# Performance work log

Hardware: AMD Instinct MI355X
Metric: run time of the kernel (lower is better)

The kernel has to match this reference:

```python
import jax, jax.numpy as jnp
import numpy as np

KSIZE = 7       # patch size
STRIDE_Q = 4    # stride_1: query patch stride
STRIDE_KV = 1   # stride_2: key/value patch stride
SCALE = 10.0    # softmax_scale


def unfold(x, k, stride, pad):
    """torch.nn.Unfold equivalent. x:[B,C,H,W] -> [B, C*k*k, L] (c-major, then kh, kw)."""
    x = jnp.pad(x, ((0, 0), (0, 0), (pad, pad), (pad, pad)))
    B, C, Hp, Wp = x.shape
    nh = (Hp - k) // stride + 1
    nw = (Wp - k) // stride + 1
    sl = lambda i, n: slice(i, i + (n - 1) * stride + 1, stride)
    # [B, C, k*k, nh, nw]
    pat = jnp.stack([x[:, :, sl(i, nh), sl(j, nw)] for i in range(k) for j in range(k)], axis=2)
    return pat.reshape(B, C * k * k, nh * nw)


def fold(p, k, stride, pad, H, W):
    """torch.nn.functional.fold equivalent (overlap-add). p:[B, C*k*k, L] -> [B,C,H,W]."""
    B, D, L = p.shape
    C = D // (k * k)
    nh = (H + 2 * pad - k) // stride + 1
    nw = (W + 2 * pad - k) // stride + 1
    p = p.reshape(B, C, k, k, nh, nw)
    out = jnp.zeros((B, C, H + 2 * pad, W + 2 * pad), p.dtype)
    sl = lambda i, n: slice(i, i + (n - 1) * stride + 1, stride)
    for i in range(k):
        for j in range(k):
            out = out.at[:, :, sl(i, nh), sl(j, nw)].add(p[:, :, i, j])
    return out[:, :, pad:pad + H, pad:pad + W]


def conv1x1(x, w, bias):
    # w: [out, in]
    return jnp.einsum('bihw,oi->bohw', x, w) + bias[None, :, None, None]


def setup_inputs() -> dict:
    key = jax.random.key(0)
    ks = jax.random.split(key, 9)
    B, Cin, H, W = 4, 64, 128, 128
    Cit = 16
    s_in = 1.0 / np.sqrt(Cin)
    s_it = 1.0 / np.sqrt(Cit)
    return {
        'b': jax.random.normal(ks[0], (B, Cin, H, W), jnp.float32),
        'g_w': jax.random.normal(ks[1], (Cit, Cin), jnp.float32) * s_in,
        'g_b': jax.random.normal(ks[2], (Cit,), jnp.float32) * 0.01,
        'th_w': jax.random.normal(ks[3], (Cit, Cin), jnp.float32) * s_in,
        'th_b': jax.random.normal(ks[4], (Cit,), jnp.float32) * 0.01,
        'ph_w': jax.random.normal(ks[5], (Cit, Cin), jnp.float32) * s_in,
        'ph_b': jax.random.normal(ks[6], (Cit,), jnp.float32) * 0.01,
        'o_w': jax.random.normal(ks[7], (Cin, Cit), jnp.float32) * s_it,
        'o_b': jax.random.normal(ks[8], (Cin,), jnp.float32) * 0.01,
    }


def reference(b, g_w, g_b, th_w, th_b, ph_w, ph_b, o_w, o_b):
    B, Cin, H, W = b.shape
    pad = KSIZE // 2
    b1 = conv1x1(b, g_w, g_b)      # queries source  [B,16,H,W]
    b2 = conv1x1(b, th_w, th_b)    # values source
    b3 = conv1x1(b, ph_w, ph_b)    # keys source

    Q = unfold(b1, KSIZE, STRIDE_Q, pad).transpose(0, 2, 1)   # [B, L1, D]
    K = unfold(b3, KSIZE, STRIDE_KV, pad).transpose(0, 2, 1)  # [B, L2, D]
    V = unfold(b2, KSIZE, STRIDE_KV, pad).transpose(0, 2, 1)  # [B, L2, D]

    scores = jnp.einsum('bqd,bkd->bqk', Q, K)                 # [B, L1, L2]
    attn = jax.nn.softmax(scores * SCALE, axis=-1)
    Zp = jnp.einsum('bqk,bkd->bqd', attn, V).transpose(0, 2, 1)  # [B, D, L1]

    y = fold(Zp, KSIZE, STRIDE_Q, pad, H, W)                  # overlap-add
    Zc = fold(jnp.ones_like(Zp), KSIZE, STRIDE_Q, pad, H, W)  # overlap counts
    y = y / Zc
    y = conv1x1(y, o_w, o_b)
    return b + y
```

## Files before the change

kernel.cpp:

```cpp
#include <hip/hip_runtime.h>
#include <math.h>

#define NB 4
#define CIN 64
#define CIT 16
#define KS 7
#define PAD 3
#define HH 128
#define WW 128
#define HP 134
#define WPS 136
#define L1 1024
#define DD 784
#define SCALE_F 10.0f
#define WSCR 4.0f
#define TCAP 128

#define NPIX (HP * WPS)
#define NHWCF (NB * NPIX * CIT)

typedef __attribute__((ext_vector_type(4))) float f32x4;
typedef __attribute__((ext_vector_type(8))) short s16x8;
typedef __attribute__((ext_vector_type(4))) unsigned int u32x4;

__device__ __forceinline__ unsigned short f2bf(float f) {
    unsigned u = __float_as_uint(f);
    unsigned r = (u + 0x7FFFu + ((u >> 16) & 1u)) >> 16;
    return (unsigned short)r;
}

__global__ __launch_bounds__(256) void k_prep(
    const float* __restrict__ bin,
    const float* __restrict__ gw, const float* __restrict__ gb,
    const float* __restrict__ tw, const float* __restrict__ tb,
    const float* __restrict__ pw, const float* __restrict__ pb,
    float* __restrict__ b1f, float* __restrict__ b2f, float* __restrict__ b3f,
    unsigned short* __restrict__ b1n, unsigned short* __restrict__ b3n)
{
    int p = blockIdx.x * 256 + threadIdx.x;
    if (p >= NB * NPIX) return;
    int x = p % WPS; int r = p / WPS; int y = r % HP; int bb = r / HP;
    bool inter = (x >= PAD && x < PAD + WW && y >= PAD && y < PAD + HH);
    float v[CIN];
    if (inter) {
        int iy = y - PAD, ix = x - PAD;
        const float* src = bin + ((size_t)(bb * CIN) * HH + iy) * WW + ix;
        #pragma unroll
        for (int ci = 0; ci < CIN; ++ci) v[ci] = src[ci * HH * WW];
    }
    float a1v[CIT], a2v[CIT], a3v[CIT];
    unsigned short o1[CIT], o3[CIT];
    #pragma unroll
    for (int co = 0; co < CIT; ++co) {
        float a1 = 0.f, a2 = 0.f, a3 = 0.f;
        if (inter) {
            a1 = gb[co]; a2 = tb[co]; a3 = pb[co];
            #pragma unroll
            for (int ci = 0; ci < CIN; ++ci) {
                float vv = v[ci];
                a1 += gw[co * CIN + ci] * vv;
                a2 += tw[co * CIN + ci] * vv;
                a3 += pw[co * CIN + ci] * vv;
            }
        }
        a1v[co] = a1; a2v[co] = a2; a3v[co] = a3;
        o1[co] = f2bf(a1); o3[co] = f2bf(a3);
    }
    size_t pb16 = (size_t)p * CIT;
    #pragma unroll
    for (int g = 0; g < 4; ++g) {
        f32x4 w1 = {a1v[4*g], a1v[4*g+1], a1v[4*g+2], a1v[4*g+3]};
        f32x4 w2 = {a2v[4*g], a2v[4*g+1], a2v[4*g+2], a2v[4*g+3]};
        f32x4 w3 = {a3v[4*g], a3v[4*g+1], a3v[4*g+2], a3v[4*g+3]};
        *(f32x4*)(b1f + pb16 + 4*g) = w1;
        *(f32x4*)(b2f + pb16 + 4*g) = w2;
        *(f32x4*)(b3f + pb16 + 4*g) = w3;
    }
    unsigned pk1[8], pk3[8];
    #pragma unroll
    for (int kk = 0; kk < 8; ++kk) {
        pk1[kk] = (unsigned)o1[2 * kk] | ((unsigned)o1[2 * kk + 1] << 16);
        pk3[kk] = (unsigned)o3[2 * kk] | ((unsigned)o3[2 * kk + 1] << 16);
    }
    unsigned short* d1 = b1n + pb16;
    unsigned short* d3 = b3n + pb16;
    u32x4 w1a = {pk1[0], pk1[1], pk1[2], pk1[3]}, w1b = {pk1[4], pk1[5], pk1[6], pk1[7]};
    u32x4 w3a = {pk3[0], pk3[1], pk3[2], pk3[3]}, w3b = {pk3[4], pk3[5], pk3[6], pk3[7]};
    *(u32x4*)d1 = w1a; *(u32x4*)(d1 + 8) = w1b;
    *(u32x4*)d3 = w3a; *(u32x4*)(d3 + 8) = w3b;
}

__global__ __launch_bounds__(512, 2) void k_screen(
    const unsigned short* __restrict__ b1n, const unsigned short* __restrict__ b3n,
    _Float16* __restrict__ tmaxh)
{
    int blk = blockIdx.x;
    int qt = blk & 3;
    int qgroup = (blk >> 2) & 63;
    int bb = blk >> 8;
    int qstart_ky = qt * 32;
    int tid = threadIdx.x;
    int lane = tid & 63, w = tid >> 6;
    int lanelow = lane & 15;
    int h = (lane >> 5) & 1;
    int clo = (lane >> 4) & 1;

    __shared__ __align__(16) short qlds[16 * 800];
    __shared__ __align__(16) short kring[8 * 134 * 16];

    const unsigned short* b1nb = b1n + (size_t)bb * (NPIX * CIT);
    const unsigned short* b3nb = b3n + (size_t)bb * (NPIX * CIT);

    int qlo = qgroup * 16;
    int qh = qlo >> 5, qw0 = qlo & 31;
    int qybase = 4 * qh;
    size_t tmbase = ((size_t)(bb * 64 + qgroup) * 4 + qt) * 4096;

    for (int task = tid; task < 800; task += 512) {
        int pp = task % 50, qq = task / 50;
        u32x4 lo = {0, 0, 0, 0}, hi = {0, 0, 0, 0};
        if (pp < 49) {
            int i = pp / 7, j = pp % 7;
            int qx = 4 * (qw0 + qq);
            const unsigned short* src = b1nb + ((size_t)(qybase + i) * WPS + qx + j) * CIT;
            lo = *(const u32x4*)src; hi = *(const u32x4*)(src + 8);
        }
        short* dst = qlds + (qq * 50 + pp) * 16;
        *(u32x4*)dst = lo; *(u32x4*)(dst + 8) = hi;
    }
    for (int task = tid; task < 8 * 268; task += 512) {
        int rr = task / 268, ch = task % 268;
        int row = qstart_ky + rr;
        *(u32x4*)(kring + rr * 2144 + ch * 8) =
            *(const u32x4*)(b3nb + (size_t)row * (WPS * CIT) + ch * 8);
    }
    __syncthreads();

    s16x8 Breg[25];
    #pragma unroll
    for (int s = 0; s < 25; ++s)
        Breg[s] = *(const s16x8*)(qlds + lanelow * 800 + s * 32 + ((lane >> 4) & 3) * 8);

    int t0 = (w & 3) * 2;
    int abase = (t0 * 16 + lanelow) * 16 + clo * 8;

    for (int it = 0; it < 16; ++it) {
        int kyb = qstart_ky + 2 * it;
        u32x4 pfA = {0, 0, 0, 0}, pfB = {0, 0, 0, 0};
        bool hasB = (tid < 24);
        if (it < 15) {
            int r1 = (tid >= 268);
            int row1 = kyb + 8 + r1;
            int ch1 = tid - r1 * 268;
            pfA = *(const u32x4*)(b3nb + (size_t)row1 * (WPS * CIT) + ch1 * 8);
            if (hasB) {
                int ch2 = tid + 512 - 268;
                pfB = *(const u32x4*)(b3nb + (size_t)(kyb + 9) * (WPS * CIT) + ch2 * 8);
            }
        }
        int kyw = kyb + (w >> 2);
        f32x4 C0 = {0.f, 0.f, 0.f, 0.f}, C1 = {0.f, 0.f, 0.f, 0.f};
        #pragma unroll
        for (int s = 0; s < 25; ++s) {
            const int pe = 2 * s;
            const int po = (2 * s + 1 < 49) ? (2 * s + 1) : 0;
            const int ie = pe / 7, je = pe % 7;
            const int io = po / 7, jo = po % 7;
            int i_h = h ? io : ie;
            int j_h = h ? jo : je;
            int slot = (kyw + i_h) & 7;
            const short* ap = kring + slot * 2144 + j_h * 16 + abase;
            s16x8 a0 = *(const s16x8*)ap;
            s16x8 a1 = *(const s16x8*)(ap + 256);
            C0 = __builtin_amdgcn_mfma_f32_16x16x32_bf16(a0, Breg[s], C0, 0, 0, 0);
            C1 = __builtin_amdgcn_mfma_f32_16x16x32_bf16(a1, Breg[s], C1, 0, 0, 0);
        }
        int kyl = 2 * it + (w >> 2);
        #pragma unroll
        for (int tt = 0; tt < 2; ++tt) {
            f32x4 C = tt ? C1 : C0;
            float lm = fmaxf(fmaxf(C[0], C[1]), fmaxf(C[2], C[3]));
            lm = fmaxf(lm, __shfl_xor(lm, 16));
            lm = fmaxf(lm, __shfl_xor(lm, 32));
            if (lane < 16)
                tmaxh[tmbase + (size_t)kyl * 128 + (t0 + tt) * 16 + lane] = (_Float16)lm;
        }
        __syncthreads();
        if (it < 15) {
            int r1 = (tid >= 268);
            int row1 = kyb + 8 + r1;
            int ch1 = tid - r1 * 268;
            *(u32x4*)(kring + (row1 & 7) * 2144 + ch1 * 8) = pfA;
            if (hasB)
                *(u32x4*)(kring + ((kyb + 9) & 7) * 2144 + (tid + 512 - 268) * 8) = pfB;
        }
        __syncthreads();
    }
}

__global__ __launch_bounds__(256) void k_finalize(
    const float* __restrict__ b1f, const float* __restrict__ b2f,
    const float* __restrict__ b3f, const _Float16* __restrict__ tmaxh,
    float* __restrict__ Zp)
{
    int wv = threadIdx.x >> 6;
    int lane = threadIdx.x & 63;
    int gq = blockIdx.x * 4 + wv;
    int bb = gq >> 10, q = gq & 1023;
    int qh = q >> 5, qw = q & 31;
    int qy = qh * 4, qx = qw * 4;
    int qidx = q & 15;
    int ch = lane & 15, pbase = lane >> 4;

    __shared__ int tq[4][TCAP];

    const float* b1b = b1f + (size_t)bb * (NPIX * CIT);
    const float* b2b = b2f + (size_t)bb * (NPIX * CIT);
    const float* b3b = b3f + (size_t)bb * (NPIX * CIT);

    const _Float16* tbq = tmaxh + (size_t)(bb * 64 + (q >> 4)) * 16384 + qidx;
    float tv[16]; float mg = -1e30f;
    #pragma unroll
    for (int k = 0; k < 16; ++k) {
        tv[k] = (float)tbq[16 * (lane + 64 * k)];
        mg = fmaxf(mg, tv[k]);
    }
    #pragma unroll
    for (int o = 32; o > 0; o >>= 1) mg = fmaxf(mg, __shfl_xor(mg, o));
    float thr = mg - WSCR;

    int cnt = 0;
    #pragma unroll
    for (int k = 0; k < 16; ++k) {
        bool p = (tv[k] >= thr);
        unsigned long long mk = __ballot(p);
        if (p) {
            int pos = cnt + (int)__popcll(mk & ((1ull << lane) - 1ull));
            if (pos < TCAP) tq[wv][pos] = lane + 64 * k;
        }
        cnt += (int)__popcll(mk);
    }
    int nt = min(cnt, TCAP);
    int n = nt * 16;
    __syncthreads();

    float qreg[13]; int offs[13];
    int qorg = (qy * WPS + qx) * CIT;
    #pragma unroll
    for (int k = 0; k < 13; ++k) {
        int p = pbase + 4 * k;
        if (p < 49) {
            int pi = p / 7, pj = p % 7;
            offs[k] = (pi * WPS + pj) * CIT + ch;
            qreg[k] = b1b[qorg + offs[k]];
        } else { offs[k] = 0; qreg[k] = 0.f; }
    }

    float m = -1e30f, l = 0.f, acc[13];
    #pragma unroll
    for (int k = 0; k < 13; ++k) acc[k] = 0.f;

    for (int ci0 = 0; ci0 < n; ci0 += 4) {
        int kb[4];
        #pragma unroll
        for (int u = 0; u < 4; ++u) {
            int ci = ci0 + u;
            int e = tq[wv][ci >> 4];
            int ky = (e >> 8) * 32 + ((e >> 3) & 31);
            int kx = (e & 7) * 16 + (ci & 15);
            kb[u] = (ky * WPS + kx) * CIT;
        }
        float kv[4][13], vv[4][13];
        #pragma unroll
        for (int u = 0; u < 4; ++u) {
            #pragma unroll
            for (int k = 0; k < 13; ++k) {
                kv[u][k] = b3b[kb[u] + offs[k]];
                vv[u][k] = b2b[kb[u] + offs[k]];
            }
        }
        float s[4];
        #pragma unroll
        for (int u = 0; u < 4; ++u) {
            float t = 0.f;
            #pragma unroll
            for (int k = 0; k < 13; ++k) t += qreg[k] * kv[u][k];
            #pragma unroll
            for (int o = 32; o > 0; o >>= 1) t += __shfl_xor(t, o);
            s[u] = t;
        }
        float mnew = fmaxf(m, fmaxf(fmaxf(s[0], s[1]), fmaxf(s[2], s[3])));
        float sc = __expf(SCALE_F * (m - mnew));
        float w0 = __expf(SCALE_F * (s[0] - mnew));
        float w1 = __expf(SCALE_F * (s[1] - mnew));
        float w2 = __expf(SCALE_F * (s[2] - mnew));
        float w3 = __expf(SCALE_F * (s[3] - mnew));
        l = l * sc + (w0 + w1 + w2 + w3);
        #pragma unroll
        for (int k = 0; k < 13; ++k)
            acc[k] = acc[k] * sc + w0 * vv[0][k] + w1 * vv[1][k]
                                 + w2 * vv[2][k] + w3 * vv[3][k];
        m = mnew;
    }

    float inv = (n > 0) ? (1.f / l) : 0.f;
    float* zq = Zp + (size_t)gq * DD;
    #pragma unroll
    for (int k = 0; k < 13; ++k) {
        int d = lane + 64 * k;
        if (d < DD) zq[d] = acc[k] * inv;
    }
}

__global__ __launch_bounds__(256) void k_fold(
    const float* __restrict__ bin, const float* __restrict__ ow,
    const float* __restrict__ ob, const float* __restrict__ Zp,
    float* __restrict__ outp)
{
    int p = blockIdx.x * 256 + threadIdx.x;
    if (p >= NB * HH * WW) return;
    int ox = p % WW; int r = p / WW; int oy = r % HH; int bb = r / HH;
    int yp = oy + PAD, xp = ox + PAD;
    int qh0 = (yp - 3) >> 2, qh1 = min(31, yp >> 2);
    int qw0 = (xp - 3) >> 2, qw1 = min(31, xp >> 2);
    float cnt = (float)((qh1 - qh0 + 1) * (qw1 - qw0 + 1));
    float y16[CIT];
    #pragma unroll
    for (int c = 0; c < CIT; ++c) y16[c] = 0.f;
    for (int qhh = qh0; qhh <= qh1; ++qhh) {
        int i = yp - 4 * qhh;
        for (int qww = qw0; qww <= qw1; ++qww) {
            int j = xp - 4 * qww;
            const float* zb = Zp + (size_t)((bb << 10) + qhh * 32 + qww) * DD + (i * 7 + j) * CIT;
            #pragma unroll
            for (int c = 0; c < CIT; ++c) y16[c] += zb[c];
        }
    }
    float icnt = 1.f / cnt;
    #pragma unroll
    for (int c = 0; c < CIT; ++c) y16[c] *= icnt;
    size_t oidx = ((size_t)(bb * CIN) * HH + oy) * WW + ox;
    for (int co = 0; co < CIN; ++co) {
        float a = ob[co];
        #pragma unroll
        for (int c = 0; c < CIT; ++c) a += ow[co * CIT + c] * y16[c];
        outp[oidx + (size_t)co * HH * WW] = bin[oidx + (size_t)co * HH * WW] + a;
    }
}

extern "C" void kernel_launch(void* const* d_in, const int* in_sizes, int n_in,
                              void* d_out, int out_size, void* d_ws, size_t ws_size,
                              hipStream_t stream) {
    (void)in_sizes; (void)n_in; (void)out_size; (void)ws_size;
    const float* bin = (const float*)d_in[0];
    const float* gw  = (const float*)d_in[1];
    const float* gb  = (const float*)d_in[2];
    const float* tw  = (const float*)d_in[3];
    const float* tb  = (const float*)d_in[4];
    const float* pw  = (const float*)d_in[5];
    const float* pb  = (const float*)d_in[6];
    const float* ow  = (const float*)d_in[7];
    const float* ob  = (const float*)d_in[8];

    float* outp = (float*)d_out;
    float* b3f = outp;
    float* b1f = outp + NHWCF;
    unsigned short* b3n = (unsigned short*)(outp + 2 * (size_t)NHWCF);
    unsigned short* b1n = b3n + NHWCF;

    float* ws = (float*)d_ws;
    float* b2f = ws;
    float* Zp  = ws + NHWCF;
    _Float16* tmaxh = (_Float16*)(ws + NHWCF + (size_t)NB * L1 * DD);

    hipLaunchKernelGGL(k_prep, dim3((NB * NPIX + 255) / 256), dim3(256), 0, stream,
                       bin, gw, gb, tw, tb, pw, pb, b1f, b2f, b3f, b1n, b3n);
    hipLaunchKernelGGL(k_screen, dim3(1024), dim3(512), 0, stream,
                       b1n, b3n, tmaxh);
    hipLaunchKernelGGL(k_finalize, dim3(1024), dim3(256), 0, stream,
                       b1f, b2f, b3f, tmaxh, Zp);
    hipLaunchKernelGGL(k_fold, dim3((NB * HH * WW + 255) / 256), dim3(256), 0, stream,
                       bin, ow, ob, Zp, outp);
}
```

Measured before the change: 257.4 us.

## Process two query groups per screen block to reuse key fragments

Each k_screen block now covers a full query row of 32 queries instead of 16, so the grid is halved. Each key A-fragment read from LDS feeds two MFMAs, one per query group, and the key ring is streamed one row per iteration with each wave owning a 16-column key tile. The intent is to halve both the LDS key reads and the global key-ring loads per query. The cost is twice as many query B-fragment registers (50 vectors) under the same launch bounds, which risks register spills or lower occupancy, plus a longer serial loop of 32 iterations per block.

Result: faster. 234.6 us (-8.9%).

```diff
diff --git a/kernel.cpp b/kernel.cpp
--- a/kernel.cpp
+++ b/kernel.cpp
@@ -96,8 +96,8 @@
 {
     int blk = blockIdx.x;
     int qt = blk & 3;
-    int qgroup = (blk >> 2) & 63;
-    int bb = blk >> 8;
+    int qh = (blk >> 2) & 31;
+    int bb = blk >> 7;
     int qstart_ky = qt * 32;
     int tid = threadIdx.x;
     int lane = tid & 63, w = tid >> 6;
@@ -105,29 +105,39 @@
     int h = (lane >> 5) & 1;
     int clo = (lane >> 4) & 1;
 
-    __shared__ __align__(16) short qlds[16 * 800];
-    __shared__ __align__(16) short kring[8 * 134 * 16];
+    __shared__ __align__(16) short smem[32 * 800];
 
     const unsigned short* b1nb = b1n + (size_t)bb * (NPIX * CIT);
     const unsigned short* b3nb = b3n + (size_t)bb * (NPIX * CIT);
 
-    int qlo = qgroup * 16;
-    int qh = qlo >> 5, qw0 = qlo & 31;
     int qybase = 4 * qh;
-    size_t tmbase = ((size_t)(bb * 64 + qgroup) * 4 + qt) * 4096;
-
-    for (int task = tid; task < 800; task += 512) {
+    size_t tmbase0 = ((size_t)(bb * 64 + 2 * qh) * 4 + qt) * 4096;
+    size_t tmbase1 = ((size_t)(bb * 64 + 2 * qh + 1) * 4 + qt) * 4096;
+
+    for (int task = tid; task < 1600; task += 512) {
         int pp = task % 50, qq = task / 50;
         u32x4 lo = {0, 0, 0, 0}, hi = {0, 0, 0, 0};
         if (pp < 49) {
             int i = pp / 7, j = pp % 7;
-            int qx = 4 * (qw0 + qq);
+            int qx = 4 * qq;
             const unsigned short* src = b1nb + ((size_t)(qybase + i) * WPS + qx + j) * CIT;
             lo = *(const u32x4*)src; hi = *(const u32x4*)(src + 8);
         }
-        short* dst = qlds + (qq * 50 + pp) * 16;
+        short* dst = smem + (qq * 50 + pp) * 16;
         *(u32x4*)dst = lo; *(u32x4*)(dst + 8) = hi;
     }
+    __syncthreads();
+
+    s16x8 B0[25], B1[25];
+    #pragma unroll
+    for (int s = 0; s < 25; ++s) {
+        int ko = s * 32 + ((lane >> 4) & 3) * 8;
+        B0[s] = *(const s16x8*)(smem + lanelow * 800 + ko);
+        B1[s] = *(const s16x8*)(smem + (lanelow + 16) * 800 + ko);
+    }
+    __syncthreads();
+
+    short* kring = smem;
     for (int task = tid; task < 8 * 268; task += 512) {
         int rr = task / 268, ch = task % 268;
         int row = qstart_ky + rr;
@@ -136,29 +146,15 @@
     }
     __syncthreads();
 
-    s16x8 Breg[25];
-    #pragma unroll
-    for (int s = 0; s < 25; ++s)
-        Breg[s] = *(const s16x8*)(qlds + lanelow * 800 + s * 32 + ((lane >> 4) & 3) * 8);
-
-    int t0 = (w & 3) * 2;
-    int abase = (t0 * 16 + lanelow) * 16 + clo * 8;
-
-    for (int it = 0; it < 16; ++it) {
-        int kyb = qstart_ky + 2 * it;
-        u32x4 pfA = {0, 0, 0, 0}, pfB = {0, 0, 0, 0};
-        bool hasB = (tid < 24);
-        if (it < 15) {
-            int r1 = (tid >= 268);
-            int row1 = kyb + 8 + r1;
-            int ch1 = tid - r1 * 268;
-            pfA = *(const u32x4*)(b3nb + (size_t)row1 * (WPS * CIT) + ch1 * 8);
-            if (hasB) {
-                int ch2 = tid + 512 - 268;
-                pfB = *(const u32x4*)(b3nb + (size_t)(kyb + 9) * (WPS * CIT) + ch2 * 8);
-            }
-        }
-        int kyw = kyb + (w >> 2);
+    int abase = (w * 16 + lanelow) * 16 + clo * 8;
+
+    for (int it = 0; it < 32; ++it) {
+        int ky = qstart_ky + it;
+        u32x4 pfA = {0, 0, 0, 0};
+        bool hasPf = (it < 30) && (tid < 268);
+        if (hasPf)
+            pfA = *(const u32x4*)(b3nb + (size_t)(ky + 8) * (WPS * CIT) + tid * 8);
+
         f32x4 C0 = {0.f, 0.f, 0.f, 0.f}, C1 = {0.f, 0.f, 0.f, 0.f};
         #pragma unroll
         for (int s = 0; s < 25; ++s) {
@@ -168,32 +164,25 @@
             const int io = po / 7, jo = po % 7;
             int i_h = h ? io : ie;
             int j_h = h ? jo : je;
-            int slot = (kyw + i_h) & 7;
+            int slot = (ky + i_h) & 7;
             const short* ap = kring + slot * 2144 + j_h * 16 + abase;
             s16x8 a0 = *(const s16x8*)ap;
-            s16x8 a1 = *(const s16x8*)(ap + 256);
-            C0 = __builtin_amdgcn_mfma_f32_16x16x32_bf16(a0, Breg[s], C0, 0, 0, 0);
-            C1 = __builtin_amdgcn_mfma_f32_16x16x32_bf16(a1, Breg[s], C1, 0, 0, 0);
-        }
-        int kyl = 2 * it + (w >> 2);
-        #pragma unroll
-        for (int tt = 0; tt < 2; ++tt) {
-            f32x4 C = tt ? C1 : C0;
-            float lm = fmaxf(fmaxf(C[0], C[1]), fmaxf(C[2], C[3]));
-            lm = fmaxf(lm, __shfl_xor(lm, 16));
-            lm = fmaxf(lm, __shfl_xor(lm, 32));
-            if (lane < 16)
-                tmaxh[tmbase + (size_t)kyl * 128 + (t0 + tt) * 16 + lane] = (_Float16)lm;
+            C0 = __builtin_amdgcn_mfma_f32_16x16x32_bf16(a0, B0[s], C0, 0, 0, 0);
+            C1 = __builtin_amdgcn_mfma_f32_16x16x32_bf16(a0, B1[s], C1, 0, 0, 0);
+        }
+        float lm0 = fmaxf(fmaxf(C0[0], C0[1]), fmaxf(C0[2], C0[3]));
+        lm0 = fmaxf(lm0, __shfl_xor(lm0, 16));
+        lm0 = fmaxf(lm0, __shfl_xor(lm0, 32));
+        float lm1 = fmaxf(fmaxf(C1[0], C1[1]), fmaxf(C1[2], C1[3]));
+        lm1 = fmaxf(lm1, __shfl_xor(lm1, 16));
+        lm1 = fmaxf(lm1, __shfl_xor(lm1, 32));
+        if (lane < 16) {
+            tmaxh[tmbase0 + (size_t)it * 128 + w * 16 + lane] = (_Float16)lm0;
+            tmaxh[tmbase1 + (size_t)it * 128 + w * 16 + lane] = (_Float16)lm1;
         }
         __syncthreads();
-        if (it < 15) {
-            int r1 = (tid >= 268);
-            int row1 = kyb + 8 + r1;
-            int ch1 = tid - r1 * 268;
-            *(u32x4*)(kring + (row1 & 7) * 2144 + ch1 * 8) = pfA;
-            if (hasB)
-                *(u32x4*)(kring + ((kyb + 9) & 7) * 2144 + (tid + 512 - 268) * 8) = pfB;
-        }
+        if (hasPf)
+            *(u32x4*)(kring + ((ky + 8) & 7) * 2144 + tid * 8) = pfA;
         __syncthreads();
     }
 }
@@ -375,7 +364,7 @@
 
     hipLaunchKernelGGL(k_prep, dim3((NB * NPIX + 255) / 256), dim3(256), 0, stream,
                        bin, gw, gb, tw, tb, pw, pb, b1f, b2f, b3f, b1n, b3n);
-    hipLaunchKernelGGL(k_screen, dim3(1024), dim3(512), 0, stream,
+    hipLaunchKernelGGL(k_screen, dim3(512), dim3(512), 0, stream,
                        b1n, b3n, tmaxh);
     hipLaunchKernelGGL(k_finalize, dim3(1024), dim3(256), 0, stream,
                        b1f, b2f, b3f, tmaxh, Zp);
```
